# Kernel optimization log

Measured on AMD Instinct MI355X. Metric: run time of the kernel, lower is better.

The kernel has to match this reference:

```python
import jax, jax.numpy as jnp
import numpy as np

B = 32          # batch
IH = IW = 32    # image_size
N = IH * IW     # tokens = 1024
INP = 256
OUP = 256
H = 8           # heads
D = 32          # dim_head
INNER = H * D   # 256
TABLE = (2 * IH - 1) * (2 * IW - 1)  # 3969


def _rel_index():
    # exact replica of the torch buffer construction
    coords = np.stack(np.meshgrid(np.arange(IH), np.arange(IW), indexing='ij')).reshape(2, -1)
    rel = coords[:, :, None] - coords[:, None, :]
    rel[0] += IH - 1
    rel[1] += IW - 1
    rel[0] *= 2 * IW - 1
    return (rel[0] + rel[1]).reshape(-1)  # [N*N]


def setup_inputs() -> dict:
    key = jax.random.key(0)
    k0, k1, k2, k3 = jax.random.split(key, 4)
    x = jax.random.normal(k0, (B, N, INP), jnp.float32)
    W_qkv = jax.random.normal(k1, (INP, 3 * INNER), jnp.float32) * 0.02
    bias_table = jax.random.normal(k2, (TABLE, H), jnp.float32) * 0.02
    W_out = jax.random.normal(k3, (INNER, OUP), jnp.float32) * 0.02
    b_out = jnp.zeros((OUP,), jnp.float32)
    rel_index = jnp.asarray(_rel_index(), jnp.int32)
    return {"x": x, "W_qkv": W_qkv, "bias_table": bias_table,
            "W_out": W_out, "b_out": b_out, "rel_index": rel_index}


def reference(x, W_qkv, bias_table, W_out, b_out, rel_index):
    scale = D ** -0.5
    qkv = x @ W_qkv                                   # [B, N, 3*INNER]
    q, k, v = jnp.split(qkv, 3, axis=-1)
    to_heads = lambda t: t.reshape(B, N, H, D).transpose(0, 2, 1, 3)  # b h n d
    q, k, v = to_heads(q), to_heads(k), to_heads(v)
    dots = jnp.einsum('bhid,bhjd->bhij', q, k) * scale  # [B, H, N, N]
    # gather per-head relative position bias: [N*N, H] -> [1, H, N, N]
    bias = bias_table[rel_index].reshape(N, N, H).transpose(2, 0, 1)[None]
    attn = jax.nn.softmax(dots + bias, axis=-1)
    out = jnp.einsum('bhij,bhjd->bhid', attn, v)        # [B, H, N, D]
    out = out.transpose(0, 2, 1, 3).reshape(B, N, INNER)
    return out @ W_out + b_out
```

## Files before the change

kernel.cpp:

```cpp
#include <hip/hip_runtime.h>

typedef __attribute__((ext_vector_type(4))) int            vi4;
typedef __attribute__((ext_vector_type(4))) float          vf4;
typedef __attribute__((ext_vector_type(8))) short          vs8;
typedef __attribute__((ext_vector_type(4))) short          vs4;
typedef __attribute__((ext_vector_type(2))) unsigned int   vu2;
typedef unsigned short u16;
typedef unsigned int   u32;

#define LOG2E  1.4426950408889634f
#define QSCALE 0.2550484109f

static __device__ __forceinline__ u16 f2bf(float f) {
  u32 u = __builtin_bit_cast(u32, f);
  u32 r = (u + 0x7fffu + ((u >> 16) & 1u)) >> 16;
  return (u16)r;
}
static __device__ __forceinline__ float bfu_lo(u32 u) {
  return __builtin_bit_cast(float, u << 16);
}
static __device__ __forceinline__ float bfu_hi(u32 u) {
  return __builtin_bit_cast(float, u & 0xffff0000u);
}
static __device__ __forceinline__ u32 packbf_perm(float a, float b) {
  return __builtin_amdgcn_perm(__builtin_bit_cast(u32, b),
                               __builtin_bit_cast(u32, a), 0x07060302u);
}
static __device__ __forceinline__ vf4 unpack_bias(const u32* grp, int tj) {
  u32 b0 = grp[tj * 2], b1 = grp[tj * 2 + 1];
  vf4 c; c[0] = bfu_lo(b0); c[1] = bfu_hi(b0);
  c[2] = bfu_lo(b1); c[3] = bfu_hi(b1);
  return c;
}
static __device__ __forceinline__ float exp2_raw(float x) {
#if __has_builtin(__builtin_amdgcn_exp2f)
  return __builtin_amdgcn_exp2f(x);
#else
  float r;
  asm("v_exp_f32 %0, %1" : "=v"(r) : "v"(x));
  return r;
#endif
}

static __device__ __forceinline__ void ldsdma16(void* lds, const void* g) {
  __builtin_amdgcn_global_load_lds(
      (const u32 __attribute__((address_space(1)))*)g,
      (u32 __attribute__((address_space(3)))*)lds, 16, 0, 0);
}

__global__ void prep_all(const float* __restrict__ x, u16* __restrict__ xbf,
                         const float* __restrict__ Wqkv, u16* __restrict__ WqkvT,
                         const float* __restrict__ Wout, u16* __restrict__ WoutT,
                         const int* __restrict__ rel, const float* __restrict__ table,
                         u32* __restrict__ bias_pk, float* __restrict__ bias_f,
                         int use_f32) {
  __shared__ __align__(8) u16 relS[64 * 32];
  int bid = blockIdx.x, tid = threadIdx.x;
  if (bid < 8192) {
    int i = (bid * 256 + tid) * 4;
    vf4 v = *(const vf4*)&x[i];
    u32 lo = (u32)f2bf(v[0]) | ((u32)f2bf(v[1]) << 16);
    u32 hi = (u32)f2bf(v[2]) | ((u32)f2bf(v[3]) << 16);
    vu2 o; o[0] = lo; o[1] = hi;
    *(vu2*)&xbf[i] = o;
  } else if (bid < 9216) {
    const float* src; u16* dst; int C, idx;
    if (bid < 8960) { src = Wqkv; dst = WqkvT; C = 768; idx = (bid - 8192) * 256 + tid; }
    else            { src = Wout; dst = WoutT; C = 256; idx = (bid - 8960) * 256 + tid; }
    int r = idx / C, c = idx - r * C;
    dst[c * 256 + r] = f2bf(src[idx]);
  } else {
    int b2 = bid - 9216;
    int qt = b2 >> 6, t = (b2 >> 2) & 15, s = b2 & 3;
    int ti = s >> 1, jhalf = s & 1;
    int wave = tid >> 6, quad = (tid >> 4) & 3, l15 = tid & 15;
    int jbase = t * 64 + jhalf * 32;

#pragma unroll
    for (int p = 0; p < 2; ++p) {
      int task = p * 256 + tid;
      int q = task >> 3, unit = task & 7;
      int m = qt * 128 + (q >> 4) * 32 + ti * 16 + (q & 15);
      vi4 v = *(const vi4*)&rel[m * 1024 + jbase + unit * 4];
      vu2 pk;
      pk[0] = (u32)(v[0] & 0xffff) | ((u32)v[1] << 16);
      pk[1] = (u32)(v[2] & 0xffff) | ((u32)v[3] << 16);
      *(vu2*)&relS[q * 32 + unit * 4] = pk;
    }
    __syncthreads();

    int mrow = wave * 16 + l15;
    float vals[8][8];
#pragma unroll
    for (int tjl = 0; tjl < 2; ++tjl)
#pragma unroll
      for (int r = 0; r < 4; ++r) {
        int idx = relS[mrow * 32 + tjl * 16 + quad * 4 + r];
        vf4 a = *(const vf4*)&table[idx * 8];
        vf4 bb = *(const vf4*)&table[idx * 8 + 4];
#pragma unroll
        for (int h = 0; h < 4; ++h) {
          vals[tjl * 4 + r][h] = a[h];
          vals[tjl * 4 + r][h + 4] = bb[h];
        }
      }
    if (use_f32) {
#pragma unroll
      for (int h = 0; h < 8; ++h)
#pragma unroll
        for (int tjl = 0; tjl < 2; ++tjl) {
          int frag = ti * 4 + jhalf * 2 + tjl;
          vf4 v;
#pragma unroll
          for (int r = 0; r < 4; ++r) v[r] = vals[tjl * 4 + r][h] * LOG2E;
          *(vf4*)&bias_f[(((h * 8 + qt) * 16 + t) * 8 + frag) * 1024 + tid * 4] = v;
        }
    } else {
#pragma unroll
      for (int h = 0; h < 8; ++h) {
        u32 o[4];
#pragma unroll
        for (int tjl = 0; tjl < 2; ++tjl)
#pragma unroll
          for (int p = 0; p < 2; ++p) {
            u32 lo = f2bf(vals[tjl * 4 + 2 * p][h] * LOG2E);
            u32 hi = f2bf(vals[tjl * 4 + 2 * p + 1][h] * LOG2E);
            o[tjl * 2 + p] = lo | (hi << 16);
          }
        *(vi4*)&bias_pk[h * 524288 + (qt * 16 + t) * 4096 + s * 1024 + tid * 4] =
            *(const vi4*)o;
      }
    }
  }
}

template <int EPI>
__global__ __launch_bounds__(256, 2) void gemm_k256(
    const u16* __restrict__ A, const u16* __restrict__ Bt,
    u16* __restrict__ q_out, u16* __restrict__ k_out, u16* __restrict__ v_out,
    float* __restrict__ c_out, const float* __restrict__ bias) {
  __shared__ __align__(16) u16 SMEM[EPI == 0 ? 128 * 136 : 8192];
  u16* As = SMEM;
  u16* Bs = SMEM + 4096;
  const int tid = threadIdx.x;
  const int lane15 = tid & 15, quad = (tid >> 4) & 3, wave = tid >> 6;
  const int wr = (wave & 1) * 64, wc = (wave >> 1) * 64;
  const int m0 = blockIdx.y * 128, n0 = blockIdx.x * 128;

  const u16* Ag = &A[(m0 + (tid >> 2)) * 256 + (tid & 3) * 8];
  const u16* Bg = &Bt[(n0 + (tid >> 2)) * 256 + (tid & 3) * 8];
  u16* AsW = &As[wave * 512];
  u16* BsW = &Bs[wave * 512];

  const vf4 z4 = {0.f, 0.f, 0.f, 0.f};
  vf4 acc[4][4];
#pragma unroll
  for (int i = 0; i < 4; ++i)
#pragma unroll
    for (int j = 0; j < 4; ++j) acc[i][j] = z4;

  for (int k0 = 0; k0 < 256; k0 += 32) {
    __syncthreads();
    ldsdma16(AsW,        Ag + k0);
    ldsdma16(AsW + 2048, Ag + k0 + 64 * 256);
    ldsdma16(BsW,        Bg + k0);
    ldsdma16(BsW + 2048, Bg + k0 + 64 * 256);
    __syncthreads();
    vs8 af[4], bfr[4];
#pragma unroll
    for (int ti = 0; ti < 4; ++ti)
      af[ti] = *(const vs8*)&As[(wr + ti * 16 + lane15) * 32 + quad * 8];
#pragma unroll
    for (int tj = 0; tj < 4; ++tj)
      bfr[tj] = *(const vs8*)&Bs[(wc + tj * 16 + lane15) * 32 + quad * 8];
#pragma unroll
    for (int ti = 0; ti < 4; ++ti)
#pragma unroll
      for (int tj = 0; tj < 4; ++tj)
        acc[ti][tj] = __builtin_amdgcn_mfma_f32_16x16x32_bf16(af[ti], bfr[tj],
                                                              acc[ti][tj], 0, 0, 0);
  }

  if (EPI == 0) {
    const int which = n0 >> 8;
    const int bb = m0 >> 10, nn0 = m0 & 1023;
    u16* Cs = SMEM;
    __syncthreads();
    if (which < 2) {
      float sc = (which == 0) ? QSCALE : 1.f;
#pragma unroll
      for (int tj = 0; tj < 4; ++tj) {
        int col = wc + tj * 16 + lane15;
#pragma unroll
        for (int ti = 0; ti < 4; ++ti) {
          int row0 = wr + ti * 16 + quad * 4;
#pragma unroll
          for (int r = 0; r < 4; ++r)
            Cs[(row0 + r) * 136 + col] = f2bf(acc[ti][tj][r] * sc);
        }
      }
      __syncthreads();
      u16* base = (which == 0) ? q_out : k_out;
#pragma unroll
      for (int hp = 0; hp < 4; ++hp) {
        int hh = ((n0 + hp * 32) >> 5) & 7;
        u16* pb = base + ((bb * 8 + hh) * 1024 + nn0) * 32;
#pragma unroll
        for (int p2 = 0; p2 < 2; ++p2) {
          int task = p2 * 256 + tid;
          int row = task >> 2, unit = task & 3;
          vi4 v = *(const vi4*)&Cs[row * 136 + hp * 32 + unit * 8];
          *(vi4*)&pb[row * 32 + unit * 8] = v;
        }
      }
    } else {
#pragma unroll
      for (int tj = 0; tj < 4; ++tj) {
        int col = wc + tj * 16 + lane15;
#pragma unroll
        for (int ti = 0; ti < 4; ++ti) {
          int row0 = wr + ti * 16 + quad * 4;
          vu2 pk;
          pk[0] = (u32)f2bf(acc[ti][tj][0]) | ((u32)f2bf(acc[ti][tj][1]) << 16);
          pk[1] = (u32)f2bf(acc[ti][tj][2]) | ((u32)f2bf(acc[ti][tj][3]) << 16);
          *(vu2*)&Cs[col * 136 + row0] = pk;
        }
      }
      __syncthreads();
#pragma unroll
      for (int p = 0; p < 8; ++p) {
        int task = p * 256 + tid;
        int col = task >> 4, unit = task & 15;
        int cg = n0 + col;
        int hh = (cg >> 5) & 7, d = cg & 31;
        vi4 v = *(const vi4*)&Cs[col * 136 + unit * 8];
        *(vi4*)&v_out[((bb * 8 + hh) * 32 + d) * 1024 + nn0 + unit * 8] = v;
      }
    }
  } else {
#pragma unroll
    for (int tj = 0; tj < 4; ++tj) {
      int colg = n0 + wc + tj * 16 + lane15;
      float bo = bias[colg];
#pragma unroll
      for (int ti = 0; ti < 4; ++ti)
#pragma unroll
        for (int r = 0; r < 4; ++r) {
          int rowg = m0 + wr + ti * 16 + quad * 4 + r;
          c_out[rowg * 256 + colg] = acc[ti][tj][r] + bo;
        }
    }
  }
}

template <int BF32>
__global__ __launch_bounds__(256, 4) void flash_attn(
    const u16* __restrict__ Qws, const u16* __restrict__ Kws,
    const u16* __restrict__ Vtws, const void* __restrict__ biasv,
    u16* __restrict__ Ows) {
  __shared__ __align__(16) u16 Ks[2][64 * 40];
  __shared__ __align__(16) u16 Vt[2][32 * 72];

  const int tid = threadIdx.x;
  const int l15 = tid & 15, quad = (tid >> 4) & 3, wave = tid >> 6;
  const int bid = blockIdx.x;
  const int h = bid & 7, b = (bid >> 3) & 31, qt = bid >> 8;
  const int q0 = qt * 128;
  const int bh = b * 8 + h;
  const u16* Qbase = Qws + (bh * 1024 + q0) * 32;
  const u16* Kbase = Kws + bh * 1024 * 32;
  const u16* Vbase = Vtws + bh * 32 * 1024;
  const float* Bf = (const float*)biasv + (h * 8 + qt) * 131072 + tid * 4;
  const u32*  Bpk = (const u32*)biasv + h * 524288 + qt * 65536 + tid * 4;

  const int kv_j = tid >> 2, kv_seg = (tid & 3) * 8;
  const int v_d = tid >> 3,  v_seg = (tid & 7) * 8;
  const u16* Kg = Kbase + kv_j * 32 + kv_seg;
  const u16* Vg = Vbase + v_d * 1024 + v_seg;

  vs8 af[2];
#pragma unroll
  for (int ti = 0; ti < 2; ++ti)
    af[ti] = *(const vs8*)&Qbase[(wave * 32 + ti * 16 + l15) * 32 + quad * 8];

  vi4 kreg = *(const vi4*)Kg;
  vi4 vreg = *(const vi4*)Vg;
  *(vi4*)&Ks[0][kv_j * 40 + kv_seg] = kreg;
  *(vi4*)&Vt[0][v_d * 72 + v_seg] = vreg;

  vf4 b0pre[4];
  vi4 bpk_pre[2];
  if (BF32) {
#pragma unroll
    for (int i = 0; i < 4; ++i) b0pre[i] = *(const vf4*)&Bf[i * 1024];
  } else {
#pragma unroll
    for (int i = 0; i < 2; ++i) bpk_pre[i] = *(const vi4*)(Bpk + i * 1024);
  }

  const vf4 z4 = {0.f, 0.f, 0.f, 0.f};
  vf4 O[2][2];
  O[0][0] = z4; O[0][1] = z4; O[1][0] = z4; O[1][1] = z4;
  vf4 Lacc[2];
  Lacc[0] = z4; Lacc[1] = z4;

  vs4 ones4;
#pragma unroll
  for (int i = 0; i < 4; ++i) ones4[i] = (short)0x3F80;

  const int ks_off = l15 * 40 + quad * 8;
  const int vt_off = l15 * 72 + quad * 4;

#define FA_TILE(T, CUR)                                                        \
  do {                                                                         \
    __syncthreads();                 \
          \
                                 \
    vf4 b1cur[4];                                                              \
    vi4 bpk1[2];                                                               \
    if (BF32) {                                                                \
      _Pragma("unroll")                                                        \
      for (int i = 0; i < 4; ++i)                                              \
        b1cur[i] = *(const vf4*)&Bf[((T) * 8 + 4 + i) * 1024];                 \
    } else {                                                                   \
      bpk1[0] = *(const vi4*)(Bpk + (T) * 4096 + 2048);                        \
      bpk1[1] = *(const vi4*)(Bpk + (T) * 4096 + 3072);                        \
    }                                                                          \
    if ((T) < 15) {                                                            \
      kreg = *(const vi4*)(Kg + ((T) + 1) * 2048);                             \
      vreg = *(const vi4*)(Vg + ((T) + 1) * 64);                               \
    }                                                                          \
    __builtin_amdgcn_s_setprio(1);                                             \
    _Pragma("unroll")                                                          \
    for (int tj = 0; tj < 4; ++tj) {                                           \
      vs8 bk = *(const vs8*)&Ks[CUR][tj * 640 + ks_off];                       \
      vs4 va0 = *(const vs4*)&Vt[CUR][vt_off + tj * 16];                       \
      vs4 va1 = *(const vs4*)&Vt[CUR][vt_off + 1152 + tj * 16];                \
      _Pragma("unroll")                                                        \
      for (int ti = 0; ti < 2; ++ti) {                                         \
        vf4 c = BF32 ? (ti ? b1cur[tj] : b0pre[tj])                            \
                     : unpack_bias((const u32*)(ti ? bpk1 : bpk_pre), tj);     \
        vf4 st = __builtin_amdgcn_mfma_f32_16x16x32_bf16(bk, af[ti], c,        \
                                                         0, 0, 0);             \
        float p0 = exp2_raw(st[0]);                                            \
        float p1 = exp2_raw(st[1]);                                            \
        float p2 = exp2_raw(st[2]);                                            \
        float p3 = exp2_raw(st[3]);                                            \
        vu2 pw; pw[0] = packbf_perm(p0, p1); pw[1] = packbf_perm(p2, p3);      \
        vs4 pf = __builtin_bit_cast(vs4, pw);                                  \
        O[ti][0] = __builtin_amdgcn_mfma_f32_16x16x16bf16_1k(va0, pf,          \
                                                             O[ti][0], 0, 0, 0); \
        O[ti][1] = __builtin_amdgcn_mfma_f32_16x16x16bf16_1k(va1, pf,          \
                                                             O[ti][1], 0, 0, 0); \
        Lacc[ti] = __builtin_amdgcn_mfma_f32_16x16x16bf16_1k(ones4, pf,        \
                                                             Lacc[ti], 0, 0, 0); \
      }                                                                        \
    }                                                                          \
    __builtin_amdgcn_s_setprio(0);                                             \
       \
    if ((T) < 15) {                                                            \
      *(vi4*)&Ks[(CUR) ^ 1][kv_j * 40 + kv_seg] = kreg;                        \
      *(vi4*)&Vt[(CUR) ^ 1][v_d * 72 + v_seg] = vreg;                          \
      if (BF32) {                                                              \
        _Pragma("unroll")                                                      \
        for (int i = 0; i < 4; ++i)                                            \
          b0pre[i] = *(const vf4*)&Bf[(((T) + 1) * 8 + i) * 1024];             \
      } else {                                                                 \
        bpk_pre[0] = *(const vi4*)(Bpk + ((T) + 1) * 4096);                    \
        bpk_pre[1] = *(const vi4*)(Bpk + ((T) + 1) * 4096 + 1024);             \
      }                                                                        \
    }                                                                          \
  } while (0)

  for (int tt = 0; tt < 16; tt += 2) {
    FA_TILE(tt, 0);
    FA_TILE(tt + 1, 1);
  }
#undef FA_TILE

#pragma unroll
  for (int ti = 0; ti < 2; ++ti) {
    float inv = __builtin_amdgcn_rcpf(Lacc[ti][0]);
    int m = q0 + wave * 32 + ti * 16 + l15;
    int rowbase = (b * 1024 + m) * 256 + h * 32;
#pragma unroll
    for (int tj2 = 0; tj2 < 2; ++tj2) {
      u32 lo = (u32)f2bf(O[ti][tj2][0] * inv) | ((u32)f2bf(O[ti][tj2][1] * inv) << 16);
      u32 hi = (u32)f2bf(O[ti][tj2][2] * inv) | ((u32)f2bf(O[ti][tj2][3] * inv) << 16);
      vu2 pk; pk[0] = lo; pk[1] = hi;
      *(vu2*)&Ows[rowbase + tj2 * 16 + quad * 4] = pk;
    }
  }
}

extern "C" void kernel_launch(void* const* d_in, const int* in_sizes, int n_in,
                              void* d_out, int out_size, void* d_ws, size_t ws_size,
                              hipStream_t stream) {
  (void)in_sizes; (void)n_in; (void)out_size;
  const float* x     = (const float*)d_in[0];
  const float* Wqkv  = (const float*)d_in[1];
  const float* table = (const float*)d_in[2];
  const float* Wout  = (const float*)d_in[3];
  const float* bout  = (const float*)d_in[4];
  const int*   rel   = (const int*)d_in[5];
  float* out = (float*)d_out;

  const int use_f32 = 0;
  const size_t bias_bytes = 16777216ull;

  char* ws = (char*)d_ws;
  u16* xbf    = (u16*)(ws);
  u16* Qws    = (u16*)(ws + 16777216);
  u16* Kws    = (u16*)(ws + 33554432);
  u16* Vtws   = (u16*)(ws + 50331648);
  void* biasp = (void*)(ws + 67108864);
  u16* WqkvT  = (u16*)(ws + 67108864 + bias_bytes);
  u16* WoutT  = WqkvT + 196608;

  prep_all<<<9728, 256, 0, stream>>>(x, xbf, Wqkv, WqkvT, Wout, WoutT,
                                     rel, table, (u32*)biasp, (float*)biasp,
                                     use_f32);
  gemm_k256<0><<<dim3(6, 256), 256, 0, stream>>>(xbf, WqkvT, Qws, Kws, Vtws,
                                                 nullptr, nullptr);
  flash_attn<0><<<2048, 256, 0, stream>>>(Qws, Kws, Vtws, biasp, xbf);
  gemm_k256<1><<<dim3(2, 256), 256, 0, stream>>>(xbf, WoutT,
                                                 nullptr, nullptr, nullptr, out, bout);
}
```

Measured before the change: 203.5 us.

## Double-buffer LDS in K=256 GEMMs and remap block indices for XCD locality

The projection GEMMs now use two LDS buffers, so the async global-to-LDS copy of the next K-slice is issued while MFMAs run on the current one, with explicit vmcnt waits and raw barriers. The grid becomes one-dimensional and block IDs are remapped so consecutive M tiles land on the same XCD (bid&7). This is meant to hide global load latency and improve L2 reuse. The cost is double the LDS for the EPI==1 variant and hand-placed waitcnt logic that must match the number of outstanding DMA ops.

```diff
diff --git a/kernel.cpp b/kernel.cpp
--- a/kernel.cpp
+++ b/kernel.cpp
@@ -139,18 +139,21 @@
     const u16* __restrict__ A, const u16* __restrict__ Bt,
     u16* __restrict__ q_out, u16* __restrict__ k_out, u16* __restrict__ v_out,
     float* __restrict__ c_out, const float* __restrict__ bias) {
-  __shared__ __align__(16) u16 SMEM[EPI == 0 ? 128 * 136 : 8192];
-  u16* As = SMEM;
-  u16* Bs = SMEM + 4096;
+  __shared__ __align__(16) u16 SMEM[EPI == 0 ? 128 * 136 : 16384];
   const int tid = threadIdx.x;
   const int lane15 = tid & 15, quad = (tid >> 4) & 3, wave = tid >> 6;
   const int wr = (wave & 1) * 64, wc = (wave >> 1) * 64;
-  const int m0 = blockIdx.y * 128, n0 = blockIdx.x * 128;
+  const int bid = blockIdx.x;
+  const int w = bid >> 3;
+  const int m0 = (((bid & 7) << 5) + (w & 31)) * 128;
+  const int n0 = (w >> 5) * 128;
 
   const u16* Ag = &A[(m0 + (tid >> 2)) * 256 + (tid & 3) * 8];
   const u16* Bg = &Bt[(n0 + (tid >> 2)) * 256 + (tid & 3) * 8];
-  u16* AsW = &As[wave * 512];
-  u16* BsW = &Bs[wave * 512];
+  u16* AsW0 = &SMEM[wave * 512];
+  u16* BsW0 = &SMEM[4096 + wave * 512];
+  u16* AsW1 = &SMEM[8192 + wave * 512];
+  u16* BsW1 = &SMEM[12288 + wave * 512];
 
   const vf4 z4 = {0.f, 0.f, 0.f, 0.f};
   vf4 acc[4][4];
@@ -159,27 +162,54 @@
 #pragma unroll
     for (int j = 0; j < 4; ++j) acc[i][j] = z4;
 
-  for (int k0 = 0; k0 < 256; k0 += 32) {
-    __syncthreads();
-    ldsdma16(AsW,        Ag + k0);
-    ldsdma16(AsW + 2048, Ag + k0 + 64 * 256);
-    ldsdma16(BsW,        Bg + k0);
-    ldsdma16(BsW + 2048, Bg + k0 + 64 * 256);
-    __syncthreads();
-    vs8 af[4], bfr[4];
-#pragma unroll
-    for (int ti = 0; ti < 4; ++ti)
-      af[ti] = *(const vs8*)&As[(wr + ti * 16 + lane15) * 32 + quad * 8];
-#pragma unroll
-    for (int tj = 0; tj < 4; ++tj)
-      bfr[tj] = *(const vs8*)&Bs[(wc + tj * 16 + lane15) * 32 + quad * 8];
-#pragma unroll
-    for (int ti = 0; ti < 4; ++ti)
-#pragma unroll
-      for (int tj = 0; tj < 4; ++tj)
-        acc[ti][tj] = __builtin_amdgcn_mfma_f32_16x16x32_bf16(af[ti], bfr[tj],
-                                                              acc[ti][tj], 0, 0, 0);
-  }
+  ldsdma16(AsW0,        Ag);
+  ldsdma16(AsW0 + 2048, Ag + 64 * 256);
+  ldsdma16(BsW0,        Bg);
+  ldsdma16(BsW0 + 2048, Bg + 64 * 256);
+
+#define G_TILE(KS, CUR)                                                        \
+  do {                                                                         \
+    if ((KS) < 7) {                                                            \
+      u16* da = (CUR) ? AsW0 : AsW1;          \
+      u16* db = (CUR) ? BsW0 : BsW1;                                           \
+      ldsdma16(da,        Ag + ((KS) + 1) * 32);                               \
+      ldsdma16(da + 2048, Ag + ((KS) + 1) * 32 + 64 * 256);                    \
+      ldsdma16(db,        Bg + ((KS) + 1) * 32);                               \
+      ldsdma16(db + 2048, Bg + ((KS) + 1) * 32 + 64 * 256);                    \
+      asm volatile("s_waitcnt vmcnt(4)" ::: "memory");                         \
+    } else {                                                                   \
+      asm volatile("s_waitcnt vmcnt(0)" ::: "memory");                         \
+    }                                                                          \
+    __builtin_amdgcn_sched_barrier(0);                                         \
+    __builtin_amdgcn_s_barrier();          \
+    __builtin_amdgcn_sched_barrier(0);                                         \
+    {                                                                          \
+      const u16* Ab = (CUR) ? &SMEM[8192] : &SMEM[0];                          \
+      const u16* Bb = Ab + 4096;                                               \
+      vs8 af[4], bfr[4];                                                       \
+      _Pragma("unroll")                                                        \
+      for (int ti = 0; ti < 4; ++ti)                                           \
+        af[ti] = *(const vs8*)&Ab[(wr + ti * 16 + lane15) * 32 + quad * 8];    \
+      _Pragma("unroll")                                                        \
+      for (int tj = 0; tj < 4; ++tj)                                           \
+        bfr[tj] = *(const vs8*)&Bb[(wc + tj * 16 + lane15) * 32 + quad * 8];   \
+      _Pragma("unroll")                                                        \
+      for (int ti = 0; ti < 4; ++ti)                                           \
+        _Pragma("unroll")                                                      \
+        for (int tj = 0; tj < 4; ++tj)                                         \
+          acc[ti][tj] = __builtin_amdgcn_mfma_f32_16x16x32_bf16(               \
+              af[ti], bfr[tj], acc[ti][tj], 0, 0, 0);                          \
+    }                                                                          \
+    __builtin_amdgcn_sched_barrier(0);                                         \
+    __builtin_amdgcn_s_barrier();        \
+  } while (0)
+
+#pragma unroll
+  for (int kk = 0; kk < 8; kk += 2) {
+    G_TILE(kk, 0);
+    G_TILE(kk + 1, 1);
+  }
+#undef G_TILE
 
   if (EPI == 0) {
     const int which = n0 >> 8;
@@ -420,9 +450,9 @@
   prep_all<<<9728, 256, 0, stream>>>(x, xbf, Wqkv, WqkvT, Wout, WoutT,
                                      rel, table, (u32*)biasp, (float*)biasp,
                                      use_f32);
-  gemm_k256<0><<<dim3(6, 256), 256, 0, stream>>>(xbf, WqkvT, Qws, Kws, Vtws,
-                                                 nullptr, nullptr);
+  gemm_k256<0><<<1536, 256, 0, stream>>>(xbf, WqkvT, Qws, Kws, Vtws,
+                                         nullptr, nullptr);
   flash_attn<0><<<2048, 256, 0, stream>>>(Qws, Kws, Vtws, biasp, xbf);
-  gemm_k256<1><<<dim3(2, 256), 256, 0, stream>>>(xbf, WoutT,
-                                                 nullptr, nullptr, nullptr, out, bout);
-}
+  gemm_k256<1><<<512, 256, 0, stream>>>(xbf, WoutT,
+                                        nullptr, nullptr, nullptr, out, bout);
+}
```

New measurement: 191.9 us. 1.06x faster.
